# Optimization experiments

Measured on AMD Instinct MI355X. Metric: run time of the kernel, lower is better.

The kernel has to match this reference:

```python
import jax, jax.numpy as jnp
import numpy as np

N = 100000      # nodes
E = 3200000     # edges
NG = 64         # graphs in batch
F_IN, H1, H2 = 128, 128, 64
DENSE = 16 * 8  # first_dense_neurons * second_dense_neurons
LABELS = 2


def setup_inputs() -> dict:
    key = jax.random.key(0)
    ks = jax.random.split(key, 12)
    x = jax.random.normal(ks[0], (N, F_IN), dtype=jnp.float32)
    edge_index = jax.random.randint(ks[1], (2, E), 0, N, dtype=jnp.int32)
    batch = jnp.sort(jax.random.randint(ks[2], (N,), 0, NG, dtype=jnp.int32))
    s = 0.05
    W1 = jax.random.normal(ks[3], (F_IN, H1), dtype=jnp.float32) * s
    b1 = jnp.zeros((H1,), dtype=jnp.float32)
    W2 = jax.random.normal(ks[4], (H1, H2), dtype=jnp.float32) * s
    b2 = jnp.zeros((H2,), dtype=jnp.float32)
    Wf1 = jax.random.normal(ks[5], (H2, DENSE), dtype=jnp.float32) * s
    bf1 = jnp.zeros((DENSE,), dtype=jnp.float32)
    Wf2 = jax.random.normal(ks[6], (DENSE, LABELS), dtype=jnp.float32) * s
    bf2 = jnp.zeros((LABELS,), dtype=jnp.float32)
    return {"x": x, "W1": W1, "b1": b1, "W2": W2, "b2": b2,
            "Wf1": Wf1, "bf1": bf1, "Wf2": Wf2, "bf2": bf2,
            "edge_index": edge_index, "batch": batch}


def _gcn_conv(x, W, b, src, dst, dis):
    # PyG GCNConv: h = x @ W, propagate with sym norm (self-loops included)
    h = x @ W
    coef = (dis[src] * dis[dst])[:, None]          # [E,1]
    agg = jax.ops.segment_sum(h[src] * coef, dst, num_segments=N)
    agg = agg + h * (dis * dis)[:, None]           # self-loop term
    return agg + b


def reference(x, W1, b1, W2, b2, Wf1, bf1, Wf2, bf2, edge_index, batch):
    src, dst = edge_index[0], edge_index[1]
    # degree with self-loops, symmetric normalization D^-1/2 (A+I) D^-1/2
    deg = 1.0 + jax.ops.segment_sum(jnp.ones((E,), x.dtype), dst, num_segments=N)
    dis = jax.lax.rsqrt(deg)
    h1 = jax.nn.relu(_gcn_conv(x, W1, b1, src, dst, dis))
    h2 = jax.nn.relu(_gcn_conv(h1, W2, b2, src, dst, dis))
    a1 = h2 @ Wf1 + bf1                            # [N, DENSE] (dropout: eval mode)
    counts = jax.ops.segment_sum(jnp.ones((N,), x.dtype), batch, num_segments=NG)
    graph_embedding = jax.ops.segment_sum(a1, batch, num_segments=NG) / jnp.maximum(counts, 1.0)[:, None]
    ic_predictions = graph_embedding @ Wf2 + bf2   # [NG, LABELS]
    penalty = jnp.float32(0.0)
    return (graph_embedding, penalty, ic_predictions)
```

## Files before the change

kernel.cpp:

```cpp
#include <hip/hip_runtime.h>


typedef __attribute__((ext_vector_type(8))) short bfrag;
typedef __attribute__((ext_vector_type(16))) float f32x16;
typedef __attribute__((ext_vector_type(2))) float floatx2;

__device__ __forceinline__ unsigned short f2bf(float f) {
    unsigned int u = __builtin_bit_cast(unsigned int, f);
    u = (u + 0x7FFFu + ((u >> 16) & 1u)) >> 16;
    return (unsigned short)u;
}
__device__ __forceinline__ float bf2f(unsigned int lo16) {
    unsigned int v = lo16 << 16;
    return __builtin_bit_cast(float, v);
}
__device__ __forceinline__ unsigned char f2fp8(float f) {
    return (unsigned char)(__builtin_amdgcn_cvt_pk_fp8_f32(f, f, 0, false) & 0xFF);
}
__device__ __forceinline__ void macc8p(floatx2* a, const uint2 v, float c) {
    floatx2 cc = {c, c};
    a[0] += __builtin_amdgcn_cvt_pk_f32_fp8((int)v.x, false) * cc;
    a[1] += __builtin_amdgcn_cvt_pk_f32_fp8((int)v.x, true) * cc;
    a[2] += __builtin_amdgcn_cvt_pk_f32_fp8((int)v.y, false) * cc;
    a[3] += __builtin_amdgcn_cvt_pk_f32_fp8((int)v.y, true) * cc;
}

template <int K, int NC>
__device__ __forceinline__ void wprep_body(int bid, const float* __restrict__ W,
                                           unsigned short* __restrict__ Wf) {
    constexpr int CT = NC / 32, KT = K / 16;
    int idx = bid * 256 + threadIdx.x;
    if (idx >= KT * CT * 64) return;
    int l = idx & 63;
    int fi = idx >> 6;
    int ct = fi % CT, kt = fi / CT;
    int n = ct * 32 + (l & 31);
    int k0 = kt * 16 + 8 * (l >> 5);
    unsigned short v[8];
#pragma unroll
    for (int j = 0; j < 8; ++j) v[j] = f2bf(W[(size_t)(k0 + j) * NC + n]);
    uint4 o;
    o.x = (unsigned)v[0] | ((unsigned)v[1] << 16);
    o.y = (unsigned)v[2] | ((unsigned)v[3] << 16);
    o.z = (unsigned)v[4] | ((unsigned)v[5] << 16);
    o.w = (unsigned)v[6] | ((unsigned)v[7] << 16);
    *(uint4*)&Wf[(size_t)idx * 8] = o;
}

__global__ __launch_bounds__(256) void fusedA_kernel(const int* __restrict__ dst,
                                                     int* __restrict__ bcount, int E, int EB,
                                                     const float* __restrict__ W1,
                                                     unsigned short* __restrict__ Wp1,
                                                     const float* __restrict__ W2,
                                                     unsigned short* __restrict__ Wp2) {
    __shared__ int h[256];
    int b = blockIdx.x;
    int t = threadIdx.x;
    if (b < EB) {
        h[t] = 0;
        __syncthreads();
        int base = b * 4096;
#pragma unroll
        for (int i = 0; i < 16; ++i) {
            int e = base + t + i * 256;
            if (e < E) atomicAdd(&h[dst[e] >> 9], 1);
        }
        __syncthreads();
        if (h[t] > 0) atomicAdd(&bcount[t], h[t]);
    } else if (b < EB + 8) {
        wprep_body<128, 128>(b - EB, W1, Wp1);
    } else {
        wprep_body<128, 64>(b - EB - 8, W2, Wp2);
    }
}

__global__ __launch_bounds__(256) void bucket_scatter_kernel(const int* __restrict__ src,
                                                             const int* __restrict__ dst,
                                                             const int* __restrict__ bcount,
                                                             int* __restrict__ bfill,
                                                             unsigned int* __restrict__ stage,
                                                             int E) {
    __shared__ int sc[256];
    __shared__ int hist[256];
    __shared__ int abase[256];
    int t = threadIdx.x;
    int bc = bcount[t];
    sc[t] = bc;
    __syncthreads();
    for (int off = 1; off < 256; off <<= 1) {
        int tmp = 0;
        if (t >= off) tmp = sc[t - off];
        __syncthreads();
        sc[t] += tmp;
        __syncthreads();
    }
    int bstart_t = sc[t] - bc;
    hist[t] = 0;
    __syncthreads();
    int base = blockIdx.x * 4096;
    int dcache[16];
#pragma unroll
    for (int i = 0; i < 16; ++i) {
        int e = base + t + i * 256;
        dcache[i] = (e < E) ? dst[e] : -1;
        if (dcache[i] >= 0) atomicAdd(&hist[dcache[i] >> 9], 1);
    }
    __syncthreads();
    if (hist[t] > 0) {
        int r = atomicAdd(&bfill[t], hist[t]);
        abase[t] = bstart_t + r;
    }
    __syncthreads();
    hist[t] = 0;
    __syncthreads();
#pragma unroll
    for (int i = 0; i < 16; ++i) {
        int e = base + t + i * 256;
        int d = dcache[i];
        if (d >= 0) {
            int b = d >> 9;
            int slot = atomicAdd(&hist[b], 1);
            stage[abase[b] + slot] = (unsigned)src[e] | ((unsigned)(d & 511) << 17);
        }
    }
}

#define SCAP 14336
__device__ __forceinline__ void csr_build_body(int b, const unsigned int* __restrict__ stage,
                                               const int* __restrict__ bcount,
                                               int* __restrict__ rowstart,
                                               float* __restrict__ dis,
                                               int* __restrict__ csr_src,
                                               int N, int NB, int E) {
    __shared__ int sc[256];
    __shared__ int cnt[512];
    __shared__ int ofs[512];
    __shared__ int psum[256];
    __shared__ unsigned int sedge[SCAP];
    int t = threadIdx.x;
    int bc = bcount[t];
    sc[t] = bc;
    __syncthreads();
    for (int off = 1; off < 256; off <<= 1) {
        int tmp = 0;
        if (t >= off) tmp = sc[t - off];
        __syncthreads();
        sc[t] += tmp;
        __syncthreads();
    }
    int ee = sc[b];
    int eb = ee - bcount[b];
    if (b == NB - 1 && t == 0) rowstart[N] = E;
    int node0 = b << 9;
    int nb = min(512, N - node0);
    cnt[t] = 0;
    cnt[t + 256] = 0;
    __syncthreads();
    for (int e = eb + t; e < ee; e += 256) {
        unsigned w = stage[e];
        int le = e - eb;
        if (le < SCAP) sedge[le] = w;
        atomicAdd(&cnt[w >> 17], 1);
    }
    __syncthreads();
    int a = cnt[2 * t], c = cnt[2 * t + 1];
    int ps = a + c;
    psum[t] = ps;
    __syncthreads();
    for (int off = 1; off < 256; off <<= 1) {
        int tmp = 0;
        if (t >= off) tmp = psum[t - off];
        __syncthreads();
        psum[t] += tmp;
        __syncthreads();
    }
    int ex = psum[t] - ps;
    ofs[2 * t] = ex;
    ofs[2 * t + 1] = ex + a;
    if (2 * t < nb) {
        rowstart[node0 + 2 * t] = eb + ex;
        dis[node0 + 2 * t] = rsqrtf(1.f + (float)a);
    }
    if (2 * t + 1 < nb) {
        rowstart[node0 + 2 * t + 1] = eb + ex + a;
        dis[node0 + 2 * t + 1] = rsqrtf(1.f + (float)c);
    }
    __syncthreads();
    for (int e = eb + t; e < ee; e += 256) {
        int le = e - eb;
        unsigned w = (le < SCAP) ? sedge[le] : stage[e];
        int l = w >> 17;
        int slot = atomicAdd(&ofs[l], 1);
        csr_src[eb + slot] = (int)(w & 0x1FFFFu);
    }
}

template <int K, int NC, bool IN_F32>
__device__ __forceinline__ void gemm_body(int gb, const void* __restrict__ Av,
                                          const unsigned short* __restrict__ Wf,
                                          unsigned char* __restrict__ C, int M) {
    constexpr int KT = K / 16, CT = NC / 32;
    int wid = gb * 4 + (int)(threadIdx.x >> 6);
    int lane = threadIdx.x & 63;
    int row0 = wid * 32;
    if (row0 >= M) return;

    bfrag B[KT][CT];
#pragma unroll
    for (int kt = 0; kt < KT; ++kt)
#pragma unroll
        for (int ct = 0; ct < CT; ++ct)
            B[kt][ct] = *(const bfrag*)&Wf[(size_t)((kt * CT + ct) * 64 + lane) * 8];

    f32x16 acc[CT];
#pragma unroll
    for (int ct = 0; ct < CT; ++ct)
#pragma unroll
        for (int i = 0; i < 16; ++i) acc[ct][i] = 0.f;

    int r = row0 + (lane & 31);
    if (r >= M) r = M - 1;
#pragma unroll
    for (int kt = 0; kt < KT; ++kt) {
        bfrag a;
        if (IN_F32) {
            const float* Arow = &((const float*)Av)[(size_t)r * K + 8 * (lane >> 5)];
            float4 v0 = *(const float4*)&Arow[kt * 16];
            float4 v1 = *(const float4*)&Arow[kt * 16 + 4];
            a[0] = (short)f2bf(v0.x); a[1] = (short)f2bf(v0.y);
            a[2] = (short)f2bf(v0.z); a[3] = (short)f2bf(v0.w);
            a[4] = (short)f2bf(v1.x); a[5] = (short)f2bf(v1.y);
            a[6] = (short)f2bf(v1.z); a[7] = (short)f2bf(v1.w);
        } else {
            const unsigned short* Arow =
                &((const unsigned short*)Av)[(size_t)r * K + 8 * (lane >> 5)];
            a = *(const bfrag*)&Arow[kt * 16];
        }
#pragma unroll
        for (int ct = 0; ct < CT; ++ct)
            acc[ct] = __builtin_amdgcn_mfma_f32_32x32x16_bf16(a, B[kt][ct], acc[ct], 0, 0, 0);
    }

    int colb = lane & 31;
    int rowq = 4 * (lane >> 5);
#pragma unroll
    for (int ct = 0; ct < CT; ++ct) {
        int col = ct * 32 + colb;
#pragma unroll
        for (int rg = 0; rg < 16; ++rg) {
            int row = row0 + (rg & 3) + 8 * (rg >> 2) + rowq;
            if (row < M) C[(size_t)row * NC + col] = f2fp8(acc[ct][rg]);
        }
    }
}

__global__ __launch_bounds__(256) void fusedB_kernel(const unsigned int* __restrict__ stage,
                                                     const int* __restrict__ bcount,
                                                     int* __restrict__ rowstart,
                                                     float* __restrict__ dis,
                                                     int* __restrict__ csr_src,
                                                     int N, int NB, int E,
                                                     const float* __restrict__ x,
                                                     const unsigned short* __restrict__ Wp1,
                                                     unsigned char* __restrict__ hf8) {
    int b = blockIdx.x;
    if (b < NB) {
        csr_build_body(b, stage, bcount, rowstart, dis, csr_src, N, NB, E);
    } else {
        gemm_body<128, 128, true>(b - NB, x, Wp1, hf8, N);
    }
}

template <int K, int NC, bool IN_F32>
__global__ __launch_bounds__(256) void gemm_mfma_kernel(const void* __restrict__ Av,
                                                        const unsigned short* __restrict__ Wf,
                                                        unsigned char* __restrict__ C,
                                                        int M) {
    gemm_body<K, NC, IN_F32>(blockIdx.x, Av, Wf, C, M);
}

template <int NC>
__global__ __launch_bounds__(256) void aggregate_kernel(const unsigned char* __restrict__ h,
                                                        const float* __restrict__ dis,
                                                        const int* __restrict__ rowstart,
                                                        const int* __restrict__ csr_src,
                                                        const float* __restrict__ bias,
                                                        unsigned short* __restrict__ out,
                                                        int N) {
    constexpr int LPR = NC / 8;
    constexpr int RPS = 64 / LPR;
    constexpr int SH = (NC == 128) ? 7 : 6;
    int wid = (blockIdx.x * blockDim.x + threadIdx.x) >> 6;
    int lane = threadIdx.x & 63;
    if (wid >= N) return;
    int n = wid;
    int sub = lane / LPR;
    int fid = lane % LPR;
    unsigned fb = (unsigned)(fid << 3);
    float d = dis[n];
    floatx2 acc2[4];
#pragma unroll
    for (int i = 0; i < 4; ++i) acc2[i] = (floatx2){0.f, 0.f};
    if (sub == 0) {
        uint2 hv = *(const uint2*)(h + (((unsigned)n << SH) | fb));
        macc8p(acc2, hv, d);
    }

    int beg = rowstart[n], end = rowstart[n + 1];
    for (int e0 = beg; e0 < end; e0 += 64) {
        int idx = e0 + lane;
        int sv = 0;
        float dv = 0.f;
        if (idx < end) {
            sv = __builtin_nontemporal_load(&csr_src[idx]);
            dv = dis[sv];
        }
        int cnt = min(64, end - e0);
        int j = 0;
        for (; j + 4 * RPS <= cnt; j += 4 * RPS) {
            int ja = j + sub, jb = j + RPS + sub, jc2 = j + 2 * RPS + sub,
                jd = j + 3 * RPS + sub;
            int sa = __shfl(sv, ja); float ca = __shfl(dv, ja);
            int sb = __shfl(sv, jb); float cb = __shfl(dv, jb);
            int sc = __shfl(sv, jc2); float cc = __shfl(dv, jc2);
            int sd = __shfl(sv, jd); float cd = __shfl(dv, jd);
            uint2 va = *(const uint2*)(h + (((unsigned)sa << SH) | fb));
            uint2 vb = *(const uint2*)(h + (((unsigned)sb << SH) | fb));
            uint2 vc = *(const uint2*)(h + (((unsigned)sc << SH) | fb));
            uint2 vd = *(const uint2*)(h + (((unsigned)sd << SH) | fb));
            macc8p(acc2, va, ca);
            macc8p(acc2, vb, cb);
            macc8p(acc2, vc, cc);
            macc8p(acc2, vd, cd);
        }
        for (; j + 2 * RPS <= cnt; j += 2 * RPS) {
            int ja = j + sub, jb = j + RPS + sub;
            int sa = __shfl(sv, ja); float ca = __shfl(dv, ja);
            int sb = __shfl(sv, jb); float cb = __shfl(dv, jb);
            uint2 va = *(const uint2*)(h + (((unsigned)sa << SH) | fb));
            uint2 vb = *(const uint2*)(h + (((unsigned)sb << SH) | fb));
            macc8p(acc2, va, ca);
            macc8p(acc2, vb, cb);
        }
        for (; j < cnt; j += RPS) {
            int jj = j + sub;
            int jc = min(jj, cnt - 1);
            int s = __shfl(sv, jc);
            float c = __shfl(dv, jc);
            if (jj >= cnt) c = 0.f;
            uint2 v = *(const uint2*)(h + (((unsigned)s << SH) | fb));
            macc8p(acc2, v, c);
        }
    }
#pragma unroll
    for (int m = LPR; m < 64; m <<= 1) {
#pragma unroll
        for (int i = 0; i < 4; ++i) {
            acc2[i].x += __shfl_xor(acc2[i].x, m);
            acc2[i].y += __shfl_xor(acc2[i].y, m);
        }
    }
    if (sub == 0) {
        const float4 bv0 = *(const float4*)&bias[fid * 8 + 0];
        const float4 bv1 = *(const float4*)&bias[fid * 8 + 4];
        float r[8];
        r[0] = fmaxf(acc2[0].x * d + bv0.x, 0.f);
        r[1] = fmaxf(acc2[0].y * d + bv0.y, 0.f);
        r[2] = fmaxf(acc2[1].x * d + bv0.z, 0.f);
        r[3] = fmaxf(acc2[1].y * d + bv0.w, 0.f);
        r[4] = fmaxf(acc2[2].x * d + bv1.x, 0.f);
        r[5] = fmaxf(acc2[2].y * d + bv1.y, 0.f);
        r[6] = fmaxf(acc2[3].x * d + bv1.z, 0.f);
        r[7] = fmaxf(acc2[3].y * d + bv1.w, 0.f);
        uint4 o;
        o.x = (unsigned)f2bf(r[0]) | ((unsigned)f2bf(r[1]) << 16);
        o.y = (unsigned)f2bf(r[2]) | ((unsigned)f2bf(r[3]) << 16);
        o.z = (unsigned)f2bf(r[4]) | ((unsigned)f2bf(r[5]) << 16);
        o.w = (unsigned)f2bf(r[6]) | ((unsigned)f2bf(r[7]) << 16);
        *(uint4*)&out[(size_t)n * NC + fid * 8] = o;
    }
}

__global__ __launch_bounds__(256) void poolcount_kernel(const unsigned short* __restrict__ h2,
                                                        const int* __restrict__ batch,
                                                        float* __restrict__ gsum,
                                                        int* __restrict__ gcnt,
                                                        int N, int PB) {
    int t = threadIdx.x;
    if ((int)blockIdx.x < PB) {
        int fid = t & 63;
        int strip = t >> 6;
        int n0 = blockIdx.x * 128;
        int nend = min(n0 + 128, N);
        int n = n0 + strip;
        if (n < nend) {
            float acc = 0.f;
            int gcur = batch[n];
            for (; n < nend; n += 4) {
                int g = batch[n];
                if (g != gcur) {
                    atomicAdd(&gsum[gcur * 64 + fid], acc);
                    acc = 0.f;
                    gcur = g;
                }
                acc += bf2f(h2[(size_t)n * 64 + fid]);
            }
            atomicAdd(&gsum[gcur * 64 + fid], acc);
        }
    } else {
        __shared__ int lc[64];
        if (t < 64) lc[t] = 0;
        __syncthreads();
        int n = ((int)blockIdx.x - PB) * 256 + t;
        if (n < N) atomicAdd(&lc[batch[n]], 1);
        __syncthreads();
        if (t < 64 && lc[t] > 0) atomicAdd(&gcnt[t], lc[t]);
    }
}

__global__ __launch_bounds__(128) void head_kernel(const float* __restrict__ gsum,
                                                   const int* __restrict__ gcnt,
                                                   const float* __restrict__ Wf1,
                                                   const float* __restrict__ bf1,
                                                   const float* __restrict__ Wf2,
                                                   const float* __restrict__ bf2,
                                                   float* __restrict__ out) {
    __shared__ float ph[64];
    __shared__ float red0[128], red1[128];
    int g = blockIdx.x, f = threadIdx.x;
    if (f < 64) ph[f] = gsum[g * 64 + f] / (float)max(gcnt[g], 1);
    __syncthreads();
    float ge = bf1[f];
#pragma unroll 8
    for (int k = 0; k < 64; ++k) ge += ph[k] * Wf1[k * 128 + f];
    out[g * 128 + f] = ge;
    red0[f] = ge * Wf2[f * 2 + 0];
    red1[f] = ge * Wf2[f * 2 + 1];
    __syncthreads();
    for (int off = 64; off > 0; off >>= 1) {
        if (f < off) { red0[f] += red0[f + off]; red1[f] += red1[f + off]; }
        __syncthreads();
    }
    if (f == 0) {
        out[8192 + 1 + g * 2 + 0] = red0[0] + bf2[0];
        out[8192 + 1 + g * 2 + 1] = red1[0] + bf2[1];
        if (g == 0) out[8192] = 0.f;
    }
}

extern "C" void kernel_launch(void* const* d_in, const int* in_sizes, int n_in,
                              void* d_out, int out_size, void* d_ws, size_t ws_size,
                              hipStream_t stream) {
    const float* x   = (const float*)d_in[0];
    const float* W1  = (const float*)d_in[1];
    const float* b1  = (const float*)d_in[2];
    const float* W2  = (const float*)d_in[3];
    const float* b2  = (const float*)d_in[4];
    const float* Wf1 = (const float*)d_in[5];
    const float* bf1 = (const float*)d_in[6];
    const float* Wf2 = (const float*)d_in[7];
    const float* bf2 = (const float*)d_in[8];
    const int* edge  = (const int*)d_in[9];
    const int* batch = (const int*)d_in[10];

    const int N = in_sizes[10];
    const int E = in_sizes[9] / 2;
    const int* srcA = edge;
    const int* dstA = edge + E;
    float* out = (float*)d_out;

    const int NB = (N + 511) >> 9;

    char* p = (char*)d_ws;
    auto alloc = [&](size_t bytes) {
        char* r = p;
        p += (bytes + 255) & ~(size_t)255;
        return r;
    };
    float* gsum     = (float*)alloc(64 * 64 * 4);
    int*   gcnt     = (int*)alloc(64 * 4);
    int*   bcount   = (int*)alloc(256 * 4);
    int*   bfill    = (int*)alloc(256 * 4);
    size_t zbytes   = (size_t)(p - (char*)d_ws);
    float* dis      = (float*)alloc((size_t)N * 4);
    int*   rowstart = (int*)alloc((size_t)(N + 1) * 4);
    unsigned short* Wp1 = (unsigned short*)alloc(8 * 4 * 64 * 8 * 2);
    unsigned short* Wp2 = (unsigned short*)alloc(8 * 2 * 64 * 8 * 2);
    unsigned int* stage = (unsigned int*)alloc((size_t)E * 4);
    int*   csr_src  = (int*)alloc((size_t)E * 4);
    unsigned char*  hf8   = (unsigned char*)alloc((size_t)N * 128);
    unsigned short* h1b   = (unsigned short*)alloc((size_t)N * 128 * 2);
    unsigned short* h2b   = (unsigned short*)alloc((size_t)N * 64 * 2);

    (void)hipMemsetAsync(d_ws, 0, zbytes, stream);

    const int EB = (E + 4095) / 4096;
    const int GB = (N + 127) / 128;
    fusedA_kernel<<<EB + 12, 256, 0, stream>>>(dstA, bcount, E, EB, W1, Wp1, W2, Wp2);
    bucket_scatter_kernel<<<EB, 256, 0, stream>>>(srcA, dstA, bcount, bfill, stage, E);
    fusedB_kernel<<<NB + GB, 256, 0, stream>>>(stage, bcount, rowstart, dis, csr_src,
                                               N, NB, E, x, Wp1, hf8);
    aggregate_kernel<128><<<(N + 3) / 4, 256, 0, stream>>>(hf8, dis, rowstart, csr_src,
                                                           b1, h1b, N);
    gemm_mfma_kernel<128, 64, false><<<GB, 256, 0, stream>>>(h1b, Wp2, hf8, N);
    aggregate_kernel<64><<<(N + 3) / 4, 256, 0, stream>>>(hf8, dis, rowstart, csr_src,
                                                          b2, h2b, N);
    const int PB = (N + 127) / 128;
    const int CB = (N + 255) / 256;
    poolcount_kernel<<<PB + CB, 256, 0, stream>>>(h2b, batch, gsum, gcnt, N, PB);
    head_kernel<<<64, 128, 0, stream>>>(gsum, gcnt, Wf1, bf1, Wf2, bf2, out);
}
```

Measured before the change: 377.6 us.

## Merge launches into cooperative kernels with grid-wide syncs

Replaces the memset, bucket-count kernel and bucket-scatter kernel with one cooperative kernel that zeroes buffers, counts, grid-syncs, then scatters, keeping the dst values in registers between phases. Likewise merges pooling/counting with the head kernel through a grid sync. The aim is to cut launch gaps and a reread of dst. It relies on the whole grid (EB+12 ≈ 794 blocks, and PB+CB ≈ 1173 blocks) being co-resident. If co-residency fails, the cooperative launch errors and its return value is ignored.

Result: slower. 630.9 us (+67.1%).

```diff
diff --git a/kernel.cpp b/kernel.cpp
--- a/kernel.cpp
+++ b/kernel.cpp
@@ -1,4 +1,7 @@
 #include <hip/hip_runtime.h>
+#include <hip/hip_cooperative_groups.h>
+
+namespace cg = cooperative_groups;
 
 
 typedef __attribute__((ext_vector_type(8))) short bfrag;
@@ -47,80 +50,75 @@
     *(uint4*)&Wf[(size_t)idx * 8] = o;
 }
 
-__global__ __launch_bounds__(256) void fusedA_kernel(const int* __restrict__ dst,
-                                                     int* __restrict__ bcount, int E, int EB,
-                                                     const float* __restrict__ W1,
-                                                     unsigned short* __restrict__ Wp1,
-                                                     const float* __restrict__ W2,
-                                                     unsigned short* __restrict__ Wp2) {
-    __shared__ int h[256];
-    int b = blockIdx.x;
-    int t = threadIdx.x;
+__global__ __launch_bounds__(256) void coopA_kernel(
+    const int* __restrict__ src, const int* __restrict__ dst,
+    int* __restrict__ bcount, int* __restrict__ bfill,
+    float* __restrict__ gsum, int* __restrict__ gcnt,
+    unsigned int* __restrict__ stage, int* __restrict__ rowstart,
+    const float* __restrict__ W1, unsigned short* __restrict__ Wp1,
+    const float* __restrict__ W2, unsigned short* __restrict__ Wp2,
+    int E, int EB, int N) {
+    cg::grid_group grid = cg::this_grid();
+    __shared__ int sc[256];
+    __shared__ int hist[256];
+    __shared__ int abase[256];
+    int b = blockIdx.x, t = threadIdx.x;
+    int gid = b * 256 + t;
+    if (gid < 4096) gsum[gid] = 0.f;
+    else if (gid < 4160) gcnt[gid - 4096] = 0;
+    else if (gid < 4416) bcount[gid - 4160] = 0;
+    else if (gid < 4672) bfill[gid - 4416] = 0;
+    if (gid == 0) rowstart[N] = E;
+    grid.sync();
+
+    int dcache[16];
+    int base = b * 4096;
     if (b < EB) {
-        h[t] = 0;
-        __syncthreads();
-        int base = b * 4096;
+        hist[t] = 0;
+        __syncthreads();
 #pragma unroll
         for (int i = 0; i < 16; ++i) {
             int e = base + t + i * 256;
-            if (e < E) atomicAdd(&h[dst[e] >> 9], 1);
-        }
-        __syncthreads();
-        if (h[t] > 0) atomicAdd(&bcount[t], h[t]);
+            dcache[i] = (e < E) ? dst[e] : -1;
+            if (dcache[i] >= 0) atomicAdd(&hist[dcache[i] >> 9], 1);
+        }
+        __syncthreads();
+        if (hist[t] > 0) atomicAdd(&bcount[t], hist[t]);
     } else if (b < EB + 8) {
         wprep_body<128, 128>(b - EB, W1, Wp1);
     } else {
         wprep_body<128, 64>(b - EB - 8, W2, Wp2);
     }
-}
-
-__global__ __launch_bounds__(256) void bucket_scatter_kernel(const int* __restrict__ src,
-                                                             const int* __restrict__ dst,
-                                                             const int* __restrict__ bcount,
-                                                             int* __restrict__ bfill,
-                                                             unsigned int* __restrict__ stage,
-                                                             int E) {
-    __shared__ int sc[256];
-    __shared__ int hist[256];
-    __shared__ int abase[256];
-    int t = threadIdx.x;
-    int bc = bcount[t];
-    sc[t] = bc;
-    __syncthreads();
-    for (int off = 1; off < 256; off <<= 1) {
-        int tmp = 0;
-        if (t >= off) tmp = sc[t - off];
-        __syncthreads();
-        sc[t] += tmp;
-        __syncthreads();
-    }
-    int bstart_t = sc[t] - bc;
-    hist[t] = 0;
-    __syncthreads();
-    int base = blockIdx.x * 4096;
-    int dcache[16];
-#pragma unroll
-    for (int i = 0; i < 16; ++i) {
-        int e = base + t + i * 256;
-        dcache[i] = (e < E) ? dst[e] : -1;
-        if (dcache[i] >= 0) atomicAdd(&hist[dcache[i] >> 9], 1);
-    }
-    __syncthreads();
-    if (hist[t] > 0) {
-        int r = atomicAdd(&bfill[t], hist[t]);
-        abase[t] = bstart_t + r;
-    }
-    __syncthreads();
-    hist[t] = 0;
-    __syncthreads();
-#pragma unroll
-    for (int i = 0; i < 16; ++i) {
-        int e = base + t + i * 256;
-        int d = dcache[i];
-        if (d >= 0) {
-            int b = d >> 9;
-            int slot = atomicAdd(&hist[b], 1);
-            stage[abase[b] + slot] = (unsigned)src[e] | ((unsigned)(d & 511) << 17);
+    grid.sync();
+
+    if (b < EB) {
+        int bc = bcount[t];
+        sc[t] = bc;
+        __syncthreads();
+        for (int off = 1; off < 256; off <<= 1) {
+            int tmp = 0;
+            if (t >= off) tmp = sc[t - off];
+            __syncthreads();
+            sc[t] += tmp;
+            __syncthreads();
+        }
+        int bstart_t = sc[t] - bc;
+        if (hist[t] > 0) {
+            int r = atomicAdd(&bfill[t], hist[t]);
+            abase[t] = bstart_t + r;
+        }
+        __syncthreads();
+        hist[t] = 0;
+        __syncthreads();
+#pragma unroll
+        for (int i = 0; i < 16; ++i) {
+            int d = dcache[i];
+            if (d >= 0) {
+                int e = base + t + i * 256;
+                int bk = d >> 9;
+                int slot = atomicAdd(&hist[bk], 1);
+                stage[abase[bk] + slot] = (unsigned)src[e] | ((unsigned)(d & 511) << 17);
+            }
         }
     }
 }
@@ -381,11 +379,20 @@
     }
 }
 
-__global__ __launch_bounds__(256) void poolcount_kernel(const unsigned short* __restrict__ h2,
-                                                        const int* __restrict__ batch,
-                                                        float* __restrict__ gsum,
-                                                        int* __restrict__ gcnt,
-                                                        int N, int PB) {
+__global__ __launch_bounds__(256) void coopB_kernel(const unsigned short* __restrict__ h2,
+                                                    const int* __restrict__ batch,
+                                                    float* __restrict__ gsum,
+                                                    int* __restrict__ gcnt,
+                                                    const float* __restrict__ Wf1,
+                                                    const float* __restrict__ bf1,
+                                                    const float* __restrict__ Wf2,
+                                                    const float* __restrict__ bf2,
+                                                    float* __restrict__ out,
+                                                    int N, int PB) {
+    cg::grid_group grid = cg::this_grid();
+    __shared__ int lc[64];
+    __shared__ float ph[64];
+    __shared__ float red0[128], red1[128];
     int t = threadIdx.x;
     if ((int)blockIdx.x < PB) {
         int fid = t & 63;
@@ -408,7 +415,6 @@
             atomicAdd(&gsum[gcur * 64 + fid], acc);
         }
     } else {
-        __shared__ int lc[64];
         if (t < 64) lc[t] = 0;
         __syncthreads();
         int n = ((int)blockIdx.x - PB) * 256 + t;
@@ -416,35 +422,29 @@
         __syncthreads();
         if (t < 64 && lc[t] > 0) atomicAdd(&gcnt[t], lc[t]);
     }
-}
-
-__global__ __launch_bounds__(128) void head_kernel(const float* __restrict__ gsum,
-                                                   const int* __restrict__ gcnt,
-                                                   const float* __restrict__ Wf1,
-                                                   const float* __restrict__ bf1,
-                                                   const float* __restrict__ Wf2,
-                                                   const float* __restrict__ bf2,
-                                                   float* __restrict__ out) {
-    __shared__ float ph[64];
-    __shared__ float red0[128], red1[128];
-    int g = blockIdx.x, f = threadIdx.x;
-    if (f < 64) ph[f] = gsum[g * 64 + f] / (float)max(gcnt[g], 1);
-    __syncthreads();
-    float ge = bf1[f];
+    grid.sync();
+    if ((int)blockIdx.x < 64) {
+        int g = blockIdx.x, f = t;
+        if (f < 64) ph[f] = gsum[g * 64 + f] / (float)max(gcnt[g], 1);
+        __syncthreads();
+        if (f < 128) {
+            float ge = bf1[f];
 #pragma unroll 8
-    for (int k = 0; k < 64; ++k) ge += ph[k] * Wf1[k * 128 + f];
-    out[g * 128 + f] = ge;
-    red0[f] = ge * Wf2[f * 2 + 0];
-    red1[f] = ge * Wf2[f * 2 + 1];
-    __syncthreads();
-    for (int off = 64; off > 0; off >>= 1) {
-        if (f < off) { red0[f] += red0[f + off]; red1[f] += red1[f + off]; }
-        __syncthreads();
-    }
-    if (f == 0) {
-        out[8192 + 1 + g * 2 + 0] = red0[0] + bf2[0];
-        out[8192 + 1 + g * 2 + 1] = red1[0] + bf2[1];
-        if (g == 0) out[8192] = 0.f;
+            for (int k = 0; k < 64; ++k) ge += ph[k] * Wf1[k * 128 + f];
+            out[g * 128 + f] = ge;
+            red0[f] = ge * Wf2[f * 2 + 0];
+            red1[f] = ge * Wf2[f * 2 + 1];
+        }
+        __syncthreads();
+        for (int off = 64; off > 0; off >>= 1) {
+            if (f < off) { red0[f] += red0[f + off]; red1[f] += red1[f + off]; }
+            __syncthreads();
+        }
+        if (f == 0) {
+            out[8192 + 1 + g * 2 + 0] = red0[0] + bf2[0];
+            out[8192 + 1 + g * 2 + 1] = red1[0] + bf2[1];
+            if (g == 0) out[8192] = 0.f;
+        }
     }
 }
 
@@ -463,8 +463,8 @@
     const int* edge  = (const int*)d_in[9];
     const int* batch = (const int*)d_in[10];
 
-    const int N = in_sizes[10];
-    const int E = in_sizes[9] / 2;
+    int N = in_sizes[10];
+    int E = in_sizes[9] / 2;
     const int* srcA = edge;
     const int* dstA = edge + E;
     float* out = (float*)d_out;
@@ -481,7 +481,6 @@
     int*   gcnt     = (int*)alloc(64 * 4);
     int*   bcount   = (int*)alloc(256 * 4);
     int*   bfill    = (int*)alloc(256 * 4);
-    size_t zbytes   = (size_t)(p - (char*)d_ws);
     float* dis      = (float*)alloc((size_t)N * 4);
     int*   rowstart = (int*)alloc((size_t)(N + 1) * 4);
     unsigned short* Wp1 = (unsigned short*)alloc(8 * 4 * 64 * 8 * 2);
@@ -492,12 +491,19 @@
     unsigned short* h1b   = (unsigned short*)alloc((size_t)N * 128 * 2);
     unsigned short* h2b   = (unsigned short*)alloc((size_t)N * 64 * 2);
 
-    (void)hipMemsetAsync(d_ws, 0, zbytes, stream);
-
-    const int EB = (E + 4095) / 4096;
+    int EB = (E + 4095) / 4096;
     const int GB = (N + 127) / 128;
-    fusedA_kernel<<<EB + 12, 256, 0, stream>>>(dstA, bcount, E, EB, W1, Wp1, W2, Wp2);
-    bucket_scatter_kernel<<<EB, 256, 0, stream>>>(srcA, dstA, bcount, bfill, stage, E);
+    int PB = (N + 127) / 128;
+    const int CB = (N + 255) / 256;
+
+    {
+        void* args[] = {(void*)&srcA, (void*)&dstA, (void*)&bcount, (void*)&bfill,
+                        (void*)&gsum, (void*)&gcnt, (void*)&stage, (void*)&rowstart,
+                        (void*)&W1, (void*)&Wp1, (void*)&W2, (void*)&Wp2,
+                        (void*)&E, (void*)&EB, (void*)&N};
+        (void)hipLaunchCooperativeKernel(coopA_kernel, dim3(EB + 12), dim3(256),
+                                         args, 0u, stream);
+    }
     fusedB_kernel<<<NB + GB, 256, 0, stream>>>(stage, bcount, rowstart, dis, csr_src,
                                                N, NB, E, x, Wp1, hf8);
     aggregate_kernel<128><<<(N + 3) / 4, 256, 0, stream>>>(hf8, dis, rowstart, csr_src,
@@ -505,8 +511,11 @@
     gemm_mfma_kernel<128, 64, false><<<GB, 256, 0, stream>>>(h1b, Wp2, hf8, N);
     aggregate_kernel<64><<<(N + 3) / 4, 256, 0, stream>>>(hf8, dis, rowstart, csr_src,
                                                           b2, h2b, N);
-    const int PB = (N + 127) / 128;
-    const int CB = (N + 255) / 256;
-    poolcount_kernel<<<PB + CB, 256, 0, stream>>>(h2b, batch, gsum, gcnt, N, PB);
-    head_kernel<<<64, 128, 0, stream>>>(gsum, gcnt, Wf1, bf1, Wf2, bf2, out);
-}
+    {
+        void* args[] = {(void*)&h2b, (void*)&batch, (void*)&gsum, (void*)&gcnt,
+                        (void*)&Wf1, (void*)&bf1, (void*)&Wf2, (void*)&bf2,
+                        (void*)&out, (void*)&N, (void*)&PB};
+        (void)hipLaunchCooperativeKernel(coopB_kernel, dim3(PB + CB), dim3(256),
+                                         args, 0u, stream);
+    }
+}
```
